# Kernel tuning notes

Measured on AMD Instinct MI355X. Metric: run time of the kernel, lower is better.

Reference implementation:

```python
import jax, jax.numpy as jnp
import numpy as np

M_BITS = 8   # mantissa bits (m in BlockQuantize)
E_BITS = 8   # exponent bits (e)
GROUP_D = 64 # column-group width from group_shapes [64,64]


def bfp_quantize_2d(W, d=GROUP_D, m=M_BITS, e=E_BITS):
    """Faithful vectorized BlockQuantize2D with calculate_bias=True.
    Groups = 64-wide column blocks spanning all rows (tensor.reshape(-1,d)[start::new_width])."""
    a, b = W.shape
    nw = b // d
    # [nw, a*d]: each row is one quantization group
    blocks = W.reshape(a, nw, d).transpose(1, 0, 2).reshape(nw, a * d)
    maxv = jnp.max(jnp.abs(blocks), axis=1, keepdims=True)
    bias = 2.0 ** e - jnp.log2(maxv) + jnp.log2(2.0 - 2.0 ** (-m + 1)) - 1.0
    max_exp = 2.0 ** e - 1.0 - bias
    max_val = 2.0 ** max_exp * (1.0 + (1.0 - 2.0 ** (-m - 1)))
    sign = jnp.sign(blocks)
    absx = jnp.clip(jnp.abs(blocks), -max_val, max_val)  # lower bound negative -> no-op, as in source
    exponent = jnp.floor(jnp.log2(absx + 1e-40))
    mantissa = absx / 2.0 ** exponent                    # in [1, 2)
    group_exp = jnp.max(exponent, axis=1, keepdims=True)
    group_exp = jnp.where(group_exp + bias < 1.0, -bias, group_exp)
    # shiftTruncateInBinaryForm
    factor = 2 ** (m - 1)                                # 128
    sm = (mantissa * factor).astype(jnp.int32)           # [128, 256)
    shift = jnp.clip((group_exp - exponent).astype(jnp.int32), 0, 31)
    shifted = jnp.right_shift(sm, shift)
    safe = jnp.maximum(shifted, 1)
    bitlen = (jnp.floor(jnp.log2(safe.astype(jnp.float32))) + 1.0).astype(jnp.int32)
    mask = jnp.where(bitlen > 8, jnp.left_shift(jnp.int32(255), bitlen - 8), jnp.int32(255))
    trunc = jnp.bitwise_and(shifted, mask).astype(jnp.float32) / factor
    q = sign * trunc * 2.0 ** group_exp
    return q.reshape(nw, a, d).transpose(1, 0, 2).reshape(a, b)


def apply_rope(t, cos, sin):
    """t: [b,s,h,hd]; complex rotation on (even, odd) pairs as in apply_rotary_emb."""
    tr = t.reshape(*t.shape[:-1], -1, 2)
    te, to = tr[..., 0], tr[..., 1]
    c = cos[None, :, None, :]
    s = sin[None, :, None, :]
    oe = te * c - to * s
    oo = te * s + to * c
    return jnp.stack([oe, oo], axis=-1).reshape(t.shape)


def setup_inputs() -> dict:
    key = jax.random.key(0)
    k = jax.random.split(key, 5)
    dim, n_heads, n_kv, hd = 4096, 32, 8, 128
    b, s = 1, 2048
    x = jax.random.normal(k[0], (b, s, dim), jnp.float32)
    wq = jax.random.normal(k[1], (n_heads * hd, dim), jnp.float32) * 0.02
    wk = jax.random.normal(k[2], (n_kv * hd, dim), jnp.float32) * 0.02
    wv = jax.random.normal(k[3], (n_kv * hd, dim), jnp.float32) * 0.02
    wo = jax.random.normal(k[4], (dim, n_heads * hd), jnp.float32) * 0.02
    inv_freq = 1.0 / (10000.0 ** (jnp.arange(0, hd, 2, dtype=jnp.float32) / hd))
    ang = jnp.outer(jnp.arange(s, dtype=jnp.float32), inv_freq)  # [s, hd/2]
    return {"x": x, "wq": wq, "wk": wk, "wv": wv, "wo": wo,
            "freqs_cos": jnp.cos(ang), "freqs_sin": jnp.sin(ang)}


def reference(x, wq, wk, wv, wo, freqs_cos, freqs_sin):
    b, s, dim = x.shape
    n_heads, n_kv, hd = 32, 8, 128
    n_rep = n_heads // n_kv
    # block-floating-point quantization of projection weights (per-64-column groups)
    wq_q = bfp_quantize_2d(wq)
    wk_q = bfp_quantize_2d(wk)
    wv_q = bfp_quantize_2d(wv)
    wo_q = bfp_quantize_2d(wo)
    q = jnp.einsum('bsd,od->bso', x, wq_q).reshape(b, s, n_heads, hd)
    kk = jnp.einsum('bsd,od->bso', x, wk_q).reshape(b, s, n_kv, hd)
    v = jnp.einsum('bsd,od->bso', x, wv_q).reshape(b, s, n_kv, hd)
    q = apply_rope(q, freqs_cos, freqs_sin)
    kk = apply_rope(kk, freqs_cos, freqs_sin)
    # repeat_kv: GQA expand kv heads by n_rep
    kk = jnp.repeat(kk, n_rep, axis=2)  # [b,s,n_heads,hd]
    v = jnp.repeat(v, n_rep, axis=2)
    scores = jnp.einsum('bshd,bthd->bhst', q, kk) / jnp.sqrt(jnp.float32(hd))
    causal = jnp.triu(jnp.full((s, s), -jnp.inf, dtype=scores.dtype), k=1)
    probs = jax.nn.softmax(scores + causal, axis=-1)
    out = jnp.einsum('bhst,bthd->bshd', probs, v).reshape(b, s, n_heads * hd)
    return jnp.einsum('bso,do->bsd', out, wo_q)
```

## Files before the change

### kernel.cpp

```cpp
#include <hip/hip_runtime.h>
#include <hip/hip_bf16.h>

typedef __hip_bfloat16 hbf16;
typedef __bf16 bf16x8 __attribute__((ext_vector_type(8)));
typedef float f32x4 __attribute__((ext_vector_type(4)));

#define MFMA16(a, b, c) __builtin_amdgcn_mfma_f32_16x16x32_bf16((a), (b), (c), 0, 0, 0)

#define ASYNC16(ldsaddr, gaddr)                                                        \
  __builtin_amdgcn_global_load_lds(                                                    \
      (__attribute__((address_space(1))) void*)(void*)(gaddr),                         \
      (__attribute__((address_space(3))) void*)(ldsaddr), 16, 0, 0)

__global__ void init_gmax_kernel(unsigned int* g) { g[threadIdx.x] = 0u; }

__global__ void quant_max_kernel(const float* __restrict__ W, unsigned int* __restrict__ gmax,
                                 int slotBase, int rowsPerSplit) {
  const int tid = threadIdx.x;
  const int group = blockIdx.x & 63;
  const int split = blockIdx.x >> 6;
  const int c4 = (tid & 15) * 4;
  const int rs = tid >> 4;
  const float* base = W + (size_t)(split * rowsPerSplit) * 4096 + group * 64 + c4;
  float m = 0.f;
  for (int r = rs; r < rowsPerSplit; r += 16) {
    float4 v = *(const float4*)(base + (size_t)r * 4096);
    m = fmaxf(m, fmaxf(fmaxf(fabsf(v.x), fabsf(v.y)), fmaxf(fabsf(v.z), fabsf(v.w))));
  }
  for (int d = 1; d < 64; d <<= 1) m = fmaxf(m, __shfl_xor(m, d, 64));
  __shared__ float wm_[4];
  if ((tid & 63) == 0) wm_[tid >> 6] = m;
  __syncthreads();
  if (tid == 0) {
    m = fmaxf(fmaxf(wm_[0], wm_[1]), fmaxf(wm_[2], wm_[3]));
    atomicMax(gmax + slotBase + group, __float_as_uint(m));
  }
}

__global__ void quant_apply_kernel(const float* __restrict__ W, hbf16* __restrict__ Wq,
                                   const unsigned int* __restrict__ gmax, int slotBase, int n4) {
  const int stride = gridDim.x * 256;
  for (int idx = blockIdx.x * 256 + threadIdx.x; idx < n4; idx += stride) {
    int col4 = idx & 1023;
    int group = col4 >> 4;
    unsigned int mb = gmax[slotBase + group];
    int gex = (int)((mb >> 23) & 255) - 127;
    float s = __uint_as_float((unsigned)(134 - gex) << 23);
    float inv = __uint_as_float((unsigned)(120 + gex) << 23);
    float4 w = *(const float4*)(W + (size_t)idx * 4);
    hbf16 t[4];
    t[0] = __float2bfloat16(truncf(w.x * s) * inv);
    t[1] = __float2bfloat16(truncf(w.y * s) * inv);
    t[2] = __float2bfloat16(truncf(w.z * s) * inv);
    t[3] = __float2bfloat16(truncf(w.w * s) * inv);
    *(uint2*)(Wq + (size_t)idx * 4) = *(uint2*)t;
  }
}

__global__ void cvt_bf16_kernel(const float* __restrict__ X, hbf16* __restrict__ Y, int n4) {
  const int stride = gridDim.x * 256;
  for (int idx = blockIdx.x * 256 + threadIdx.x; idx < n4; idx += stride) {
    float4 v = *(const float4*)(X + (size_t)idx * 4);
    hbf16 t[4] = {__float2bfloat16(v.x), __float2bfloat16(v.y),
                  __float2bfloat16(v.z), __float2bfloat16(v.w)};
    *(uint2*)(Y + (size_t)idx * 4) = *(uint2*)t;
  }
}

__global__ void rope_kernel(const float* __restrict__ In, const float* __restrict__ Cs,
                            const float* __restrict__ Sn, hbf16* __restrict__ Out,
                            int shift, int rowStride) {
  int i = blockIdx.x * 256 + threadIdx.x;
  int ppr = 1 << shift;
  if (i >= 2048 * ppr) return;
  int s = i >> shift;
  int p = i & (ppr - 1);
  int t = p & 63;
  float2 q = *(const float2*)(In + (size_t)s * rowStride + p * 2);
  float c = Cs[s * 64 + t], sn = Sn[s * 64 + t];
  hbf16 o[2] = {__float2bfloat16(q.x * c - q.y * sn), __float2bfloat16(q.x * sn + q.y * c)};
  *(unsigned int*)(Out + (size_t)s * ppr * 2 + p * 2) = *(unsigned int*)o;
}

__global__ void transpose_v_kernel(const float* __restrict__ KV, hbf16* __restrict__ Vt) {
  __shared__ float tile[64][65];
  const int g = blockIdx.x, sb = blockIdx.y, db = blockIdx.z;
  const int tid = threadIdx.x;
  const int c = tid & 63;
  for (int r = tid >> 6; r < 64; r += 4)
    tile[r][c] = KV[(size_t)(sb * 64 + r) * 2048 + 1024 + g * 128 + db * 64 + c];
  __syncthreads();
  for (int r = tid >> 6; r < 64; r += 4)
    Vt[(size_t)g * 262144 + (size_t)(db * 64 + r) * 2048 + sb * 64 + c] =
        __float2bfloat16(tile[c][r]);
}

__global__ __launch_bounds__(256) void gemm_bt_kernel(const hbf16* __restrict__ A,
                                                      const hbf16* __restrict__ Bt,
                                                      float* __restrict__ C, int N) {
  constexpr int K = 4096;
  __shared__ __align__(16) hbf16 sA[128 * 64];
  __shared__ __align__(16) hbf16 sB[128 * 64];
  const int tid = threadIdx.x;
  const int wave = tid >> 6, lane = tid & 63;
  const int l15 = lane & 15, quad = lane >> 4;
  const int bm = blockIdx.x, bn = blockIdx.y;
  const int wm = (wave >> 1) * 64, wn = (wave & 1) * 64;

  const char* Ab = (const char*)(A + (size_t)bm * 128 * K);
  const char* Bb = (const char*)(Bt + (size_t)bn * 128 * K);
  char* sAb = (char*)sA;
  char* sBb = (char*)sB;

  f32x4 acc[4][4];
#pragma unroll
  for (int i = 0; i < 4; ++i)
#pragma unroll
    for (int n = 0; n < 4; ++n) acc[i][n] = (f32x4){0.f, 0.f, 0.f, 0.f};

  for (int kk = 0; kk < K; kk += 64) {
#pragma unroll
    for (int r = 0; r < 4; ++r) {
      int f = r * 4096 + tid * 16;
      int row = f >> 7;
      int lc = ((f >> 4) & 7) ^ (row & 7);
      ASYNC16(sAb + f, Ab + (size_t)row * (K * 2) + kk * 2 + lc * 16);
      ASYNC16(sBb + f, Bb + (size_t)row * (K * 2) + kk * 2 + lc * 16);
    }
    __syncthreads();
#pragma unroll
    for (int kc = 0; kc < 2; ++kc) {
      bf16x8 af[4], bg[4];
#pragma unroll
      for (int i = 0; i < 4; ++i)
        af[i] = *(const bf16x8*)(sAb + (wm + i * 16 + l15) * 128 +
                                 (((kc << 2) | quad) ^ (l15 & 7)) * 16);
#pragma unroll
      for (int n = 0; n < 4; ++n)
        bg[n] = *(const bf16x8*)(sBb + (wn + n * 16 + l15) * 128 +
                                 (((kc << 2) | quad) ^ (l15 & 7)) * 16);
#pragma unroll
      for (int i = 0; i < 4; ++i)
#pragma unroll
        for (int n = 0; n < 4; ++n) acc[i][n] = MFMA16(af[i], bg[n], acc[i][n]);
    }
    __syncthreads();
  }
#pragma unroll
  for (int i = 0; i < 4; ++i) {
    int row = bm * 128 + wm + i * 16 + quad * 4;
#pragma unroll
    for (int n = 0; n < 4; ++n) {
      float* cp = C + (size_t)row * N + bn * 128 + wn + n * 16 + l15;
#pragma unroll
      for (int r = 0; r < 4; ++r) cp[(size_t)r * N] = acc[i][n][r];
    }
  }
}

__global__ __launch_bounds__(256, 4) void attn_kernel(const hbf16* __restrict__ Q,
                                                      const hbf16* __restrict__ Kr,
                                                      const hbf16* __restrict__ Vt,
                                                      hbf16* __restrict__ O) {
  __shared__ __align__(16) hbf16 sK[64 * 128];
  __shared__ __align__(16) hbf16 sV[128 * 64];
  const int tid = threadIdx.x;
  const int wave = tid >> 6, lane = tid & 63;
  const int l15 = lane & 15, quad = lane >> 4;
  const int bid = blockIdx.x;
  const int h = bid >> 5;
  const int qb = (31 - (bid & 31) + 8 * (h & 3)) & 31;
  const int g = h >> 2;
  const int qrow0 = qb * 64 + wave * 16;
  const int qrow = qrow0 + l15;

  bf16x8 qf[4];
  {
    const hbf16* qp = Q + (size_t)qrow * 4096 + h * 128 + quad * 8;
#pragma unroll
    for (int kc = 0; kc < 4; ++kc) qf[kc] = *(const bf16x8*)(qp + kc * 32);
  }
  f32x4 of[8];
#pragma unroll
  for (int nf = 0; nf < 8; ++nf) of[nf] = (f32x4){0.f, 0.f, 0.f, 0.f};
  float m_i = -1e30f, l_i = 0.f;

  const char* Kb = (const char*)Kr + (size_t)g * 256;
  const char* Vb = (const char*)Vt + (size_t)g * 524288;
  char* sKb = (char*)sK;
  char* sVb = (char*)sV;
  const float kSc = 0.12753139668280277f;

  const int nkb = qb + 1;
  for (int kb = 0; kb < nkb; ++kb) {
#pragma unroll
    for (int r = 0; r < 4; ++r) {
      int f = r * 4096 + tid * 16;
      {
        int row = f >> 8;
        int lc = ((f >> 4) & 15) ^ (row & 15);
        ASYNC16(sKb + f, Kb + (size_t)(kb * 64 + row) * 2048 + lc * 16);
      }
      {
        int row = f >> 7;
        int lc = ((f >> 4) & 7) ^ (row & 7);
        ASYNC16(sVb + f, Vb + (size_t)row * 4096 + kb * 128 + lc * 16);
      }
    }
    __syncthreads();

    f32x4 sacc[4];
#pragma unroll
    for (int n = 0; n < 4; ++n) sacc[n] = (f32x4){0.f, 0.f, 0.f, 0.f};
#pragma unroll
    for (int n = 0; n < 4; ++n)
#pragma unroll
      for (int kc = 0; kc < 4; ++kc) {
        bf16x8 kf = *(const bf16x8*)(sKb + (n * 16 + l15) * 256 +
                                     (((kc << 2) | quad) ^ l15) * 16);
        sacc[n] = MFMA16(kf, qf[kc], sacc[n]);
      }

    float p[4][4];
    float mx = -1e30f;
    const int key0 = kb * 64 + quad * 4;
#pragma unroll
    for (int n = 0; n < 4; ++n)
#pragma unroll
      for (int r = 0; r < 4; ++r) {
        float s = sacc[n][r] * kSc;
        s = (key0 + n * 16 + r > qrow) ? -1e30f : s;
        p[n][r] = s;
        mx = fmaxf(mx, s);
      }
    mx = fmaxf(mx, __shfl_xor(mx, 16, 64));
    mx = fmaxf(mx, __shfl_xor(mx, 32, 64));
    float mnew = fmaxf(m_i, mx);
    float alpha = exp2f(m_i - mnew);
    m_i = mnew;
    float sum = 0.f;
#pragma unroll
    for (int n = 0; n < 4; ++n)
#pragma unroll
      for (int r = 0; r < 4; ++r) {
        p[n][r] = exp2f(p[n][r] - mnew);
        sum += p[n][r];
      }
    sum += __shfl_xor(sum, 16, 64);
    sum += __shfl_xor(sum, 32, 64);
    l_i = l_i * alpha + sum;
#pragma unroll
    for (int nf = 0; nf < 8; ++nf)
#pragma unroll
      for (int r = 0; r < 4; ++r) of[nf][r] *= alpha;

    unsigned pk[8];
#pragma unroll
    for (int n = 0; n < 4; ++n)
#pragma unroll
      for (int h2 = 0; h2 < 2; ++h2) {
        hbf16 t2[2] = {__float2bfloat16(p[n][2 * h2]), __float2bfloat16(p[n][2 * h2 + 1])};
        pk[n * 2 + h2] = *(unsigned*)t2;
      }

    const int sa = ((quad & 1) << 5) + l15;
    const int sb2 = sa + 16;
#pragma unroll
    for (int kc = 0; kc < 2; ++kc) {
      unsigned a0 = __shfl((int)pk[kc * 4 + 0], sa, 64);
      unsigned a1 = __shfl((int)pk[kc * 4 + 1], sa, 64);
      unsigned a2 = __shfl((int)pk[kc * 4 + 2], sa, 64);
      unsigned a3 = __shfl((int)pk[kc * 4 + 3], sa, 64);
      unsigned b0 = __shfl((int)pk[kc * 4 + 0], sb2, 64);
      unsigned b1 = __shfl((int)pk[kc * 4 + 1], sb2, 64);
      unsigned b2 = __shfl((int)pk[kc * 4 + 2], sb2, 64);
      unsigned b3 = __shfl((int)pk[kc * 4 + 3], sb2, 64);
      union {
        unsigned u[4];
        bf16x8 v;
      } pf;
      pf.u[0] = (quad < 2) ? a0 : a2;
      pf.u[1] = (quad < 2) ? a1 : a3;
      pf.u[2] = (quad < 2) ? b0 : b2;
      pf.u[3] = (quad < 2) ? b1 : b3;
#pragma unroll
      for (int nf = 0; nf < 8; ++nf) {
        bf16x8 vf = *(const bf16x8*)(sVb + (nf * 16 + l15) * 128 +
                                     (((kc << 2) | quad) ^ (l15 & 7)) * 16);
        of[nf] = MFMA16(vf, pf.v, of[nf]);
      }
    }
    __syncthreads();
  }

  const float invl = 1.f / l_i;
#pragma unroll
  for (int nf = 0; nf < 8; ++nf) {
    hbf16 t4[4];
#pragma unroll
    for (int r = 0; r < 4; ++r) t4[r] = __float2bfloat16(of[nf][r] * invl);
    *(uint2*)(O + (size_t)qrow * 4096 + h * 128 + nf * 16 + quad * 4) = *(uint2*)t4;
  }
}

extern "C" void kernel_launch(void* const* d_in, const int* in_sizes, int n_in,
                              void* d_out, int out_size, void* d_ws, size_t ws_size,
                              hipStream_t stream) {
  const float* x = (const float*)d_in[0];
  const float* wq = (const float*)d_in[1];
  const float* wk = (const float*)d_in[2];
  const float* wv = (const float*)d_in[3];
  const float* wo = (const float*)d_in[4];
  const float* fc = (const float*)d_in[5];
  const float* fs = (const float*)d_in[6];
  float* out = (float*)d_out;

  char* w = (char*)d_ws;
  size_t off = 0;
  auto alloc = [&](size_t bytes) -> char* {
    char* p = w + off;
    off += (bytes + 255) & ~(size_t)255;
    return p;
  };
  unsigned int* gmax = (unsigned int*)alloc(1024);
  hbf16* xb = (hbf16*)alloc((size_t)2048 * 4096 * 2);
  hbf16* wbuf1 = (hbf16*)alloc((size_t)4096 * 4096 * 2);
  hbf16* wbuf2 = (hbf16*)alloc((size_t)2048 * 4096 * 2);
  float* qf32 = (float*)alloc((size_t)2048 * 4096 * 4);
  float* kvf32 = (float*)alloc((size_t)2048 * 2048 * 4);
  hbf16* qrope = (hbf16*)alloc((size_t)2048 * 4096 * 2);
  hbf16* krope = (hbf16*)alloc((size_t)2048 * 1024 * 2);
  hbf16* vt = (hbf16*)alloc((size_t)8 * 128 * 2048 * 2);
  hbf16* attno = (hbf16*)qf32;

  init_gmax_kernel<<<1, 256, 0, stream>>>(gmax);
  quant_max_kernel<<<512, 256, 0, stream>>>(wq, gmax, 0, 512);
  quant_max_kernel<<<512, 256, 0, stream>>>(wk, gmax, 64, 128);
  quant_max_kernel<<<512, 256, 0, stream>>>(wv, gmax, 128, 128);
  quant_max_kernel<<<512, 256, 0, stream>>>(wo, gmax, 192, 512);
  quant_apply_kernel<<<2048, 256, 0, stream>>>(wq, wbuf1, gmax, 0, 4096 * 4096 / 4);
  quant_apply_kernel<<<1024, 256, 0, stream>>>(wk, wbuf2, gmax, 64, 1024 * 4096 / 4);
  quant_apply_kernel<<<1024, 256, 0, stream>>>(wv, wbuf2 + (size_t)1024 * 4096, gmax, 128,
                                               1024 * 4096 / 4);
  cvt_bf16_kernel<<<2048, 256, 0, stream>>>(x, xb, 2048 * 4096 / 4);
  gemm_bt_kernel<<<dim3(16, 32), 256, 0, stream>>>(xb, wbuf1, qf32, 4096);
  gemm_bt_kernel<<<dim3(16, 16), 256, 0, stream>>>(xb, wbuf2, kvf32, 2048);
  quant_apply_kernel<<<2048, 256, 0, stream>>>(wo, wbuf1, gmax, 192, 4096 * 4096 / 4);
  rope_kernel<<<16384, 256, 0, stream>>>(qf32, fc, fs, qrope, 11, 4096);
  rope_kernel<<<4096, 256, 0, stream>>>(kvf32, fc, fs, krope, 9, 2048);
  transpose_v_kernel<<<dim3(8, 32, 2), 256, 0, stream>>>(kvf32, vt);
  attn_kernel<<<1024, 256, 0, stream>>>(qrope, krope, vt, attno);
  gemm_bt_kernel<<<dim3(16, 32), 256, 0, stream>>>(attno, wbuf1, out, 4096);
  (void)in_sizes; (void)n_in; (void)out_size; (void)ws_size;
}
```

Measured before the change: 638.7 us.

## Fuse QKV projection into one GEMM and batch quantization launches

Concatenates the quantized Wq/Wk/Wv into a single 6144-row weight buffer so the Q and KV projections run as one GEMM launch with a fused output. Merges the four max-reduction launches and three quant-apply launches into multi-y-grid kernels. Folds the softmax scale into Q via RoPE, skips causal masking on non-diagonal key blocks, uses the hardware exp2 builtin, and changes the query-block permutation. This trades a slightly larger workspace and strided output rows for fewer launches and a better-filled GEMM grid.

```diff
diff --git a/kernel.cpp b/kernel.cpp
--- a/kernel.cpp
+++ b/kernel.cpp
@@ -12,10 +12,26 @@
       (__attribute__((address_space(1))) void*)(void*)(gaddr),                         \
       (__attribute__((address_space(3))) void*)(ldsaddr), 16, 0, 0)
 
+static __device__ __forceinline__ float fexp2(float x) {
+#if __has_builtin(__builtin_amdgcn_exp2f)
+  return __builtin_amdgcn_exp2f(x);
+#else
+  return exp2f(x);
+#endif
+}
+
 __global__ void init_gmax_kernel(unsigned int* g) { g[threadIdx.x] = 0u; }
 
-__global__ void quant_max_kernel(const float* __restrict__ W, unsigned int* __restrict__ gmax,
-                                 int slotBase, int rowsPerSplit) {
+__global__ void quant_max_kernel(const float* __restrict__ wq, const float* __restrict__ wk,
+                                 const float* __restrict__ wv, const float* __restrict__ wo,
+                                 unsigned int* __restrict__ gmax) {
+  const int my = blockIdx.y;
+  const float* W;
+  int slotBase, rowsPerSplit;
+  if (my == 0) { W = wq; slotBase = 0;   rowsPerSplit = 512; }
+  else if (my == 1) { W = wk; slotBase = 64;  rowsPerSplit = 128; }
+  else if (my == 2) { W = wv; slotBase = 128; rowsPerSplit = 128; }
+  else { W = wo; slotBase = 192; rowsPerSplit = 512; }
   const int tid = threadIdx.x;
   const int group = blockIdx.x & 63;
   const int split = blockIdx.x >> 6;
@@ -37,12 +53,12 @@
   }
 }
 
-__global__ void quant_apply_kernel(const float* __restrict__ W, hbf16* __restrict__ Wq,
-                                   const unsigned int* __restrict__ gmax, int slotBase, int n4) {
+__device__ __forceinline__ void quant_body(const float* __restrict__ W, hbf16* __restrict__ Wq,
+                                           const unsigned int* __restrict__ gmax, int slotBase,
+                                           int n4) {
   const int stride = gridDim.x * 256;
   for (int idx = blockIdx.x * 256 + threadIdx.x; idx < n4; idx += stride) {
-    int col4 = idx & 1023;
-    int group = col4 >> 4;
+    int group = (idx & 1023) >> 4;
     unsigned int mb = gmax[slotBase + group];
     int gex = (int)((mb >> 23) & 255) - 127;
     float s = __uint_as_float((unsigned)(134 - gex) << 23);
@@ -57,6 +73,20 @@
   }
 }
 
+__global__ void quant_apply_qkv_kernel(const float* __restrict__ wq, const float* __restrict__ wk,
+                                       const float* __restrict__ wv, hbf16* __restrict__ Wq,
+                                       const unsigned int* __restrict__ gmax) {
+  const int my = blockIdx.y;
+  if (my == 0) quant_body(wq, Wq, gmax, 0, 4096 * 4096 / 4);
+  else if (my == 1) quant_body(wk, Wq + (size_t)4096 * 4096, gmax, 64, 1024 * 4096 / 4);
+  else quant_body(wv, Wq + (size_t)5120 * 4096, gmax, 128, 1024 * 4096 / 4);
+}
+
+__global__ void quant_apply_kernel(const float* __restrict__ W, hbf16* __restrict__ Wq,
+                                   const unsigned int* __restrict__ gmax, int slotBase, int n4) {
+  quant_body(W, Wq, gmax, slotBase, n4);
+}
+
 __global__ void cvt_bf16_kernel(const float* __restrict__ X, hbf16* __restrict__ Y, int n4) {
   const int stride = gridDim.x * 256;
   for (int idx = blockIdx.x * 256 + threadIdx.x; idx < n4; idx += stride) {
@@ -69,7 +99,7 @@
 
 __global__ void rope_kernel(const float* __restrict__ In, const float* __restrict__ Cs,
                             const float* __restrict__ Sn, hbf16* __restrict__ Out,
-                            int shift, int rowStride) {
+                            int shift, int rowStride, float scale) {
   int i = blockIdx.x * 256 + threadIdx.x;
   int ppr = 1 << shift;
   if (i >= 2048 * ppr) return;
@@ -77,18 +107,18 @@
   int p = i & (ppr - 1);
   int t = p & 63;
   float2 q = *(const float2*)(In + (size_t)s * rowStride + p * 2);
-  float c = Cs[s * 64 + t], sn = Sn[s * 64 + t];
+  float c = Cs[s * 64 + t] * scale, sn = Sn[s * 64 + t] * scale;
   hbf16 o[2] = {__float2bfloat16(q.x * c - q.y * sn), __float2bfloat16(q.x * sn + q.y * c)};
   *(unsigned int*)(Out + (size_t)s * ppr * 2 + p * 2) = *(unsigned int*)o;
 }
 
-__global__ void transpose_v_kernel(const float* __restrict__ KV, hbf16* __restrict__ Vt) {
+__global__ void transpose_v_kernel(const float* __restrict__ QKV, hbf16* __restrict__ Vt) {
   __shared__ float tile[64][65];
   const int g = blockIdx.x, sb = blockIdx.y, db = blockIdx.z;
   const int tid = threadIdx.x;
   const int c = tid & 63;
   for (int r = tid >> 6; r < 64; r += 4)
-    tile[r][c] = KV[(size_t)(sb * 64 + r) * 2048 + 1024 + g * 128 + db * 64 + c];
+    tile[r][c] = QKV[(size_t)(sb * 64 + r) * 6144 + 5120 + g * 128 + db * 64 + c];
   __syncthreads();
   for (int r = tid >> 6; r < 64; r += 4)
     Vt[(size_t)g * 262144 + (size_t)(db * 64 + r) * 2048 + sb * 64 + c] =
@@ -169,7 +199,7 @@
   const int l15 = lane & 15, quad = lane >> 4;
   const int bid = blockIdx.x;
   const int h = bid >> 5;
-  const int qb = (31 - (bid & 31) + 8 * (h & 3)) & 31;
+  const int qb = (31 - (bid & 31) + 8 * ((bid >> 8) & 3)) & 31;
   const int g = h >> 2;
   const int qrow0 = qb * 64 + wave * 16;
   const int qrow = qrow0 + l15;
@@ -189,7 +219,6 @@
   const char* Vb = (const char*)Vt + (size_t)g * 524288;
   char* sKb = (char*)sK;
   char* sVb = (char*)sV;
-  const float kSc = 0.12753139668280277f;
 
   const int nkb = qb + 1;
   for (int kb = 0; kb < nkb; ++kb) {
@@ -223,27 +252,37 @@
 
     float p[4][4];
     float mx = -1e30f;
-    const int key0 = kb * 64 + quad * 4;
-#pragma unroll
-    for (int n = 0; n < 4; ++n)
-#pragma unroll
-      for (int r = 0; r < 4; ++r) {
-        float s = sacc[n][r] * kSc;
-        s = (key0 + n * 16 + r > qrow) ? -1e30f : s;
-        p[n][r] = s;
-        mx = fmaxf(mx, s);
-      }
+    if (kb == qb) {
+      const int key0 = kb * 64 + quad * 4;
+#pragma unroll
+      for (int n = 0; n < 4; ++n)
+#pragma unroll
+        for (int r = 0; r < 4; ++r) {
+          float s = sacc[n][r];
+          s = (key0 + n * 16 + r > qrow) ? -1e30f : s;
+          p[n][r] = s;
+          mx = fmaxf(mx, s);
+        }
+    } else {
+#pragma unroll
+      for (int n = 0; n < 4; ++n)
+#pragma unroll
+        for (int r = 0; r < 4; ++r) {
+          p[n][r] = sacc[n][r];
+          mx = fmaxf(mx, sacc[n][r]);
+        }
+    }
     mx = fmaxf(mx, __shfl_xor(mx, 16, 64));
     mx = fmaxf(mx, __shfl_xor(mx, 32, 64));
     float mnew = fmaxf(m_i, mx);
-    float alpha = exp2f(m_i - mnew);
+    float alpha = fexp2(m_i - mnew);
     m_i = mnew;
     float sum = 0.f;
 #pragma unroll
     for (int n = 0; n < 4; ++n)
 #pragma unroll
       for (int r = 0; r < 4; ++r) {
-        p[n][r] = exp2f(p[n][r] - mnew);
+        p[n][r] = fexp2(p[n][r] - mnew);
         sum += p[n][r];
       }
     sum += __shfl_xor(sum, 16, 64);
@@ -324,32 +363,26 @@
   };
   unsigned int* gmax = (unsigned int*)alloc(1024);
   hbf16* xb = (hbf16*)alloc((size_t)2048 * 4096 * 2);
-  hbf16* wbuf1 = (hbf16*)alloc((size_t)4096 * 4096 * 2);
-  hbf16* wbuf2 = (hbf16*)alloc((size_t)2048 * 4096 * 2);
-  float* qf32 = (float*)alloc((size_t)2048 * 4096 * 4);
-  float* kvf32 = (float*)alloc((size_t)2048 * 2048 * 4);
+  hbf16* wqkv = (hbf16*)alloc((size_t)6144 * 4096 * 2);
+  float* qkv = (float*)alloc((size_t)2048 * 6144 * 4);
   hbf16* qrope = (hbf16*)alloc((size_t)2048 * 4096 * 2);
   hbf16* krope = (hbf16*)alloc((size_t)2048 * 1024 * 2);
   hbf16* vt = (hbf16*)alloc((size_t)8 * 128 * 2048 * 2);
-  hbf16* attno = (hbf16*)qf32;
+  hbf16* woq = wqkv;
+  hbf16* attno = (hbf16*)qkv;
+
+  const float kSc = 0.12753139668280277f;
 
   init_gmax_kernel<<<1, 256, 0, stream>>>(gmax);
-  quant_max_kernel<<<512, 256, 0, stream>>>(wq, gmax, 0, 512);
-  quant_max_kernel<<<512, 256, 0, stream>>>(wk, gmax, 64, 128);
-  quant_max_kernel<<<512, 256, 0, stream>>>(wv, gmax, 128, 128);
-  quant_max_kernel<<<512, 256, 0, stream>>>(wo, gmax, 192, 512);
-  quant_apply_kernel<<<2048, 256, 0, stream>>>(wq, wbuf1, gmax, 0, 4096 * 4096 / 4);
-  quant_apply_kernel<<<1024, 256, 0, stream>>>(wk, wbuf2, gmax, 64, 1024 * 4096 / 4);
-  quant_apply_kernel<<<1024, 256, 0, stream>>>(wv, wbuf2 + (size_t)1024 * 4096, gmax, 128,
-                                               1024 * 4096 / 4);
+  quant_max_kernel<<<dim3(512, 4), 256, 0, stream>>>(wq, wk, wv, wo, gmax);
+  quant_apply_qkv_kernel<<<dim3(2048, 3), 256, 0, stream>>>(wq, wk, wv, wqkv, gmax);
   cvt_bf16_kernel<<<2048, 256, 0, stream>>>(x, xb, 2048 * 4096 / 4);
-  gemm_bt_kernel<<<dim3(16, 32), 256, 0, stream>>>(xb, wbuf1, qf32, 4096);
-  gemm_bt_kernel<<<dim3(16, 16), 256, 0, stream>>>(xb, wbuf2, kvf32, 2048);
-  quant_apply_kernel<<<2048, 256, 0, stream>>>(wo, wbuf1, gmax, 192, 4096 * 4096 / 4);
-  rope_kernel<<<16384, 256, 0, stream>>>(qf32, fc, fs, qrope, 11, 4096);
-  rope_kernel<<<4096, 256, 0, stream>>>(kvf32, fc, fs, krope, 9, 2048);
-  transpose_v_kernel<<<dim3(8, 32, 2), 256, 0, stream>>>(kvf32, vt);
+  gemm_bt_kernel<<<dim3(16, 48), 256, 0, stream>>>(xb, wqkv, qkv, 6144);
+  quant_apply_kernel<<<2048, 256, 0, stream>>>(wo, woq, gmax, 192, 4096 * 4096 / 4);
+  rope_kernel<<<16384, 256, 0, stream>>>(qkv, fc, fs, qrope, 11, 6144, kSc);
+  rope_kernel<<<4096, 256, 0, stream>>>(qkv + 4096, fc, fs, krope, 9, 6144, 1.0f);
+  transpose_v_kernel<<<dim3(8, 32, 2), 256, 0, stream>>>(qkv, vt);
   attn_kernel<<<1024, 256, 0, stream>>>(qrope, krope, vt, attno);
-  gemm_bt_kernel<<<dim3(16, 32), 256, 0, stream>>>(attno, wbuf1, out, 4096);
+  gemm_bt_kernel<<<dim3(16, 32), 256, 0, stream>>>(attno, woq, out, 4096);
   (void)in_sizes; (void)n_in; (void)out_size; (void)ws_size;
 }
```

Result: faster. 588.3 us (-7.9%).
